# Optimization experiments

Measured on AMD Instinct MI355X. Metric: run time of the kernel, lower is better.

Reference implementation:

```python
import jax, jax.numpy as jnp
import numpy as np


def setup_inputs() -> dict:
    key = jax.random.key(0)
    x = jax.random.normal(key, (8, 512, 96, 96), dtype=jnp.float32)
    gamma = jnp.zeros((1,), dtype=jnp.float32)  # Scale(0) learnable scalar
    return {"x": x, "gamma": gamma}


def reference(x, gamma):
    b, c, h, w = x.shape
    y = x.reshape(b, c, h * w)                      # [B, C, N]
    # channel-channel Gram matrix: [B, C, C]
    att = jnp.einsum('bcn,bdn->bcd', y, y)
    # DANet variant: softmax of (rowmax - scores)
    att = jnp.max(att, axis=-1, keepdims=True) - att
    att = jax.nn.softmax(att, axis=-1)
    # attention-weighted aggregation over channels: [B, C, N]
    feat = jnp.einsum('bcd,bdn->bcn', att, y).reshape(b, c, h, w)
    return gamma * feat + x
```

## Files before the change

kernel.cpp:

```cpp
#include <hip/hip_runtime.h>


typedef __attribute__((ext_vector_type(8))) short short8;
typedef __attribute__((ext_vector_type(4))) float f32x4;

#define GT 128
#define BK 64
#define LDA 72
#define NSPLIT 8
#define FBSPLIT 4

__device__ inline unsigned short f2bf(float f) {
    unsigned u = __builtin_bit_cast(unsigned, f);
    u += 0x7fffu + ((u >> 16) & 1u);
    return (unsigned short)(u >> 16);
}
__device__ inline unsigned permpack(float a, float b) {
    return __builtin_amdgcn_perm(__builtin_bit_cast(unsigned, b),
                                 __builtin_bit_cast(unsigned, a), 0x07060302u);
}
__device__ inline void gload_lds16(const short* g, short* l) {
    __builtin_amdgcn_global_load_lds(
        (const __attribute__((address_space(1))) void*)(g),
        (__attribute__((address_space(3))) void*)(l), 16, 0, 0);
}

__global__ __launch_bounds__(256) void tobf16_kernel(const float* __restrict__ x,
                                                     short* __restrict__ ybf) {
    const size_t total = (size_t)8 * 512 * 9216 / 8;
    const size_t stride = (size_t)gridDim.x * 256;
    for (size_t i = (size_t)blockIdx.x * 256 + threadIdx.x; i < total; i += stride) {
        const float4 a = ((const float4*)x)[2 * i];
        const float4 b = ((const float4*)x)[2 * i + 1];
        uint4 pv;
        pv.x = permpack(a.x, a.y);
        pv.y = permpack(a.z, a.w);
        pv.z = permpack(b.x, b.y);
        pv.w = permpack(b.z, b.w);
        ((uint4*)ybf)[i] = pv;
    }
}

__global__ __launch_bounds__(256, 3) void gram_kernel2(const short* __restrict__ ybf,
                                                       float* __restrict__ att) {
    const int C = 512, N = 9216;
    __shared__ short As[GT * BK];
    __shared__ short Bs[GT * BK];
    const int pair = blockIdx.x;
    const int i_ = (pair < 4) ? 0 : (pair < 7) ? 1 : (pair < 9) ? 2 : 3;
    const int j_ = pair - ((i_ == 0) ? 0 : (i_ == 1) ? 3 : (i_ == 2) ? 5 : 6);
    const int split = blockIdx.y, batch = blockIdx.z;
    const int c0 = i_ * GT, d0 = j_ * GT;
    const short* Y = ybf + (size_t)batch * C * N;
    const int t = threadIdx.x;
    const int w = t >> 6, l = t & 63;
    const int mw = (w >> 1) * 64, nw = (w & 1) * 64;
    const int lr = l & 15, lq = l >> 4;

    f32x4 acc[4][4] = {};
    const int kw = N / NSPLIT;
    const int kbeg = split * kw;
    for (int k0 = kbeg; k0 < kbeg + kw; k0 += BK) {
        #pragma unroll
        for (int p = 0; p < 4; ++p) {
            const int u = t + p * 256;
            const int row = u >> 3;
            const int us = (u ^ row) & 7;
            gload_lds16(Y + (size_t)(c0 + row) * N + k0 + us * 8, &As[u * 8]);
        }
        #pragma unroll
        for (int p = 0; p < 4; ++p) {
            const int u = t + p * 256;
            const int row = u >> 3;
            const int us = (u ^ row) & 7;
            gload_lds16(Y + (size_t)(d0 + row) * N + k0 + us * 8, &Bs[u * 8]);
        }
        __syncthreads();
        #pragma unroll
        for (int h = 0; h < 2; ++h) {
            short8 af[4], bf[4];
            #pragma unroll
            for (int i = 0; i < 4; i++) {
                const int r = mw + i * 16 + lr;
                af[i] = *(short8*)&As[r * BK + (((h * 4 + lq) ^ (r & 7)) * 8)];
            }
            #pragma unroll
            for (int j = 0; j < 4; j++) {
                const int r = nw + j * 16 + lr;
                bf[j] = *(short8*)&Bs[r * BK + (((h * 4 + lq) ^ (r & 7)) * 8)];
            }
            #pragma unroll
            for (int i = 0; i < 4; i++)
                #pragma unroll
                for (int j = 0; j < 4; j++)
                    acc[i][j] = __builtin_amdgcn_mfma_f32_16x16x32_bf16(af[i], bf[j], acc[i][j], 0, 0, 0);
        }
        __syncthreads();
    }
    float* S = att + (size_t)batch * C * C;
    const bool mirror = (i_ != j_);
    #pragma unroll
    for (int i = 0; i < 4; i++)
        #pragma unroll
        for (int j = 0; j < 4; j++)
            #pragma unroll
            for (int r = 0; r < 4; r++) {
                const int row = c0 + mw + i * 16 + lq * 4 + r;
                const int col = d0 + nw + j * 16 + lr;
                const float v = acc[i][j][r];
                unsafeAtomicAdd(&S[(size_t)row * C + col], v);
                if (mirror) unsafeAtomicAdd(&S[(size_t)col * C + row], v);
            }
}

__global__ __launch_bounds__(256) void softmax_kernel(float* __restrict__ att) {
    const int C = 512;
    float* S = att + (size_t)blockIdx.x * C;
    const int t = threadIdx.x;
    const float v0 = S[t], v1 = S[t + 256];

    float mn = fminf(v0, v1);
    #pragma unroll
    for (int off = 32; off > 0; off >>= 1) mn = fminf(mn, __shfl_xor(mn, off));
    __shared__ float redmin[4];
    const int wid = t >> 6, lane = t & 63;
    if (lane == 0) redmin[wid] = mn;
    __syncthreads();
    mn = fminf(fminf(redmin[0], redmin[1]), fminf(redmin[2], redmin[3]));

    const float e0 = expf(mn - v0), e1 = expf(mn - v1);
    float s = e0 + e1;
    #pragma unroll
    for (int off = 32; off > 0; off >>= 1) s += __shfl_xor(s, off);
    __shared__ float redsum[4];
    if (lane == 0) redsum[wid] = s;
    __syncthreads();
    s = redsum[0] + redsum[1] + redsum[2] + redsum[3];

    const float inv = 1.0f / s;
    unsigned short* S16 = (unsigned short*)S;
    S16[t] = f2bf(e0 * inv);
    S16[t + 256] = f2bf(e1 * inv);
}

__global__ __launch_bounds__(256, 3) void feat_kernel2(const float* __restrict__ att,
                                                       const short* __restrict__ ybf,
                                                       const float* __restrict__ x,
                                                       const float* __restrict__ gamma,
                                                       float* __restrict__ out) {
    const int C = 512, N = 9216;
    __shared__ short As[GT * BK];
    __shared__ short Bs[GT * BK];
    const int b  = blockIdx.z;
    const int c0 = blockIdx.y * GT;
    const int n0 = blockIdx.x * GT;
    const short* Ab = (const short*)(att + (size_t)b * C * C);
    const short* Y = ybf + (size_t)b * C * N;
    const int t = threadIdx.x;
    const int w = t >> 6, l = t & 63;
    const int mw = (w >> 1) * 64, nw = (w & 1) * 64;
    const int lr = l & 15, lq = l >> 4;
    const int ng = t & 31, kg = t >> 5;

    f32x4 acc[4][4] = {};
    for (int k0 = 0; k0 < C; k0 += BK) {
        #pragma unroll
        for (int p = 0; p < 4; ++p) {
            const int u = t + p * 256;
            const int row = u >> 3;
            const int us = (u ^ row) & 7;
            gload_lds16(Ab + (size_t)(c0 + row) * 1024 + k0 + us * 8, &As[u * 8]);
        }
        {
            const short* pB = Y + (size_t)(k0 + kg * 8) * N + n0 + ng * 4;
            uint2 rr[8];
            #pragma unroll
            for (int r = 0; r < 8; ++r) rr[r] = *(const uint2*)(pB + (size_t)r * N);
            #pragma unroll
            for (int j = 0; j < 4; ++j) {
                const unsigned sel = (j & 1) ? 0x07060302u : 0x05040100u;
                unsigned w0, w1, w2, w3;
                if (j < 2) {
                    w0 = __builtin_amdgcn_perm(rr[1].x, rr[0].x, sel);
                    w1 = __builtin_amdgcn_perm(rr[3].x, rr[2].x, sel);
                    w2 = __builtin_amdgcn_perm(rr[5].x, rr[4].x, sel);
                    w3 = __builtin_amdgcn_perm(rr[7].x, rr[6].x, sel);
                } else {
                    w0 = __builtin_amdgcn_perm(rr[1].y, rr[0].y, sel);
                    w1 = __builtin_amdgcn_perm(rr[3].y, rr[2].y, sel);
                    w2 = __builtin_amdgcn_perm(rr[5].y, rr[4].y, sel);
                    w3 = __builtin_amdgcn_perm(rr[7].y, rr[6].y, sel);
                }
                const int nrow = ng * 4 + j;
                uint4 cv; cv.x = w0; cv.y = w1; cv.z = w2; cv.w = w3;
                *(uint4*)&Bs[nrow * BK + ((kg ^ (nrow & 7)) * 8)] = cv;
            }
        }
        __syncthreads();
        #pragma unroll
        for (int h = 0; h < 2; ++h) {
            short8 af[4], bf[4];
            #pragma unroll
            for (int i = 0; i < 4; i++) {
                const int r = mw + i * 16 + lr;
                af[i] = *(short8*)&As[r * BK + (((h * 4 + lq) ^ (r & 7)) * 8)];
            }
            #pragma unroll
            for (int j = 0; j < 4; j++) {
                const int r = nw + j * 16 + lr;
                bf[j] = *(short8*)&Bs[r * BK + (((h * 4 + lq) ^ (r & 7)) * 8)];
            }
            #pragma unroll
            for (int i = 0; i < 4; i++)
                #pragma unroll
                for (int j = 0; j < 4; j++)
                    acc[i][j] = __builtin_amdgcn_mfma_f32_16x16x32_bf16(af[i], bf[j], acc[i][j], 0, 0, 0);
        }
        __syncthreads();
    }

    const float g = gamma[0];
    float* O = out + (size_t)b * C * N;
    const float* X = x + (size_t)b * C * N;
    #pragma unroll
    for (int i = 0; i < 4; i++)
        #pragma unroll
        for (int j = 0; j < 4; j++)
            #pragma unroll
            for (int r = 0; r < 4; r++) {
                const int row = c0 + mw + i * 16 + lq * 4 + r;
                const int col = n0 + nw + j * 16 + lr;
                const size_t idx = (size_t)row * N + col;
                O[idx] = g * acc[i][j][r] + X[idx];
            }
}

__global__ __launch_bounds__(256, 2) void gram_fb(const float* __restrict__ x,
                                                  float* __restrict__ att,
                                                  int C, int N) {
    __shared__ short As[GT * LDA];
    __shared__ short Bs[GT * LDA];
    const int bz = blockIdx.z;
    const int batch = bz & 7, split = bz >> 3;
    const int c0 = blockIdx.y * GT;
    const int d0 = blockIdx.x * GT;
    const float* Y = x + (size_t)batch * C * N;
    const int t = threadIdx.x;
    const int w = t >> 6, l = t & 63;
    const int mw = (w >> 1) * 64, nw = (w & 1) * 64;
    const int lr = l & 15, lq = l >> 4;

    f32x4 acc[4][4] = {};
    const int kbeg = split * (N / FBSPLIT);
    const int kend = kbeg + (N / FBSPLIT);
    for (int k0 = kbeg; k0 < kend; k0 += BK) {
        #pragma unroll
        for (int i = 0; i < 8; i++) {
            const int v = t + i * 256;
            const int row = v >> 4, kq = v & 15;
            float4 a = *(const float4*)(Y + (size_t)(c0 + row) * N + k0 + kq * 4);
            uint2 pa = make_uint2(permpack(a.x, a.y), permpack(a.z, a.w));
            *(uint2*)&As[row * LDA + kq * 4] = pa;
            float4 bv = *(const float4*)(Y + (size_t)(d0 + row) * N + k0 + kq * 4);
            uint2 pb = make_uint2(permpack(bv.x, bv.y), permpack(bv.z, bv.w));
            *(uint2*)&Bs[row * LDA + kq * 4] = pb;
        }
        __syncthreads();
        #pragma unroll
        for (int h = 0; h < 2; h++) {
            short8 af[4], bf[4];
            #pragma unroll
            for (int i = 0; i < 4; i++)
                af[i] = *(short8*)&As[(mw + i * 16 + lr) * LDA + h * 32 + lq * 8];
            #pragma unroll
            for (int j = 0; j < 4; j++)
                bf[j] = *(short8*)&Bs[(nw + j * 16 + lr) * LDA + h * 32 + lq * 8];
            #pragma unroll
            for (int i = 0; i < 4; i++)
                #pragma unroll
                for (int j = 0; j < 4; j++)
                    acc[i][j] = __builtin_amdgcn_mfma_f32_16x16x32_bf16(af[i], bf[j], acc[i][j], 0, 0, 0);
        }
        __syncthreads();
    }
    float* S = att + (size_t)batch * C * C;
    #pragma unroll
    for (int i = 0; i < 4; i++)
        #pragma unroll
        for (int j = 0; j < 4; j++)
            #pragma unroll
            for (int r = 0; r < 4; r++) {
                const int row = c0 + mw + i * 16 + lq * 4 + r;
                const int col = d0 + nw + j * 16 + lr;
                unsafeAtomicAdd(&S[(size_t)row * C + col], acc[i][j][r]);
            }
}

__global__ __launch_bounds__(256, 2) void feat_fb(const float* __restrict__ att,
                                                  const float* __restrict__ x,
                                                  const float* __restrict__ gamma,
                                                  float* __restrict__ out,
                                                  int C, int N) {
    __shared__ short As[GT * LDA];
    __shared__ short Bs[GT * LDA];
    const int b  = blockIdx.z;
    const int c0 = blockIdx.y * GT;
    const int n0 = blockIdx.x * GT;
    const short* Ab = (const short*)(att + (size_t)b * C * C);
    const float* Y = x + (size_t)b * C * N;
    const int t = threadIdx.x;
    const int w = t >> 6, l = t & 63;
    const int mw = (w >> 1) * 64, nw = (w & 1) * 64;
    const int lr = l & 15, lq = l >> 4;

    f32x4 acc[4][4] = {};
    for (int k0 = 0; k0 < C; k0 += BK) {
        #pragma unroll
        for (int i = 0; i < 4; i++) {
            const int v = t + i * 256;
            const int row = v >> 3, q = v & 7;
            uint4 va = *(const uint4*)(Ab + (size_t)(c0 + row) * 1024 + k0 + q * 8);
            *(uint4*)&As[row * LDA + q * 8] = va;
        }
        #pragma unroll
        for (int i = 0; i < 2; i++) {
            const int v = t + i * 256;
            const int kg = v & 15, ng = v >> 4;
            const float* p0 = Y + (size_t)(k0 + kg * 4) * N + n0 + ng * 4;
            float4 r0 = *(const float4*)(p0);
            float4 r1 = *(const float4*)(p0 + N);
            float4 r2 = *(const float4*)(p0 + 2 * (size_t)N);
            float4 r3 = *(const float4*)(p0 + 3 * (size_t)N);
            const float j0[4] = {r0.x, r1.x, r2.x, r3.x};
            const float j1[4] = {r0.y, r1.y, r2.y, r3.y};
            const float j2[4] = {r0.z, r1.z, r2.z, r3.z};
            const float j3[4] = {r0.w, r1.w, r2.w, r3.w};
            const float* cols[4] = {j0, j1, j2, j3};
            #pragma unroll
            for (int j = 0; j < 4; j++) {
                uint2 p = make_uint2(permpack(cols[j][0], cols[j][1]),
                                     permpack(cols[j][2], cols[j][3]));
                *(uint2*)&Bs[(ng * 4 + j) * LDA + kg * 4] = p;
            }
        }
        __syncthreads();
        #pragma unroll
        for (int h = 0; h < 2; h++) {
            short8 af[4], bf[4];
            #pragma unroll
            for (int i = 0; i < 4; i++)
                af[i] = *(short8*)&As[(mw + i * 16 + lr) * LDA + h * 32 + lq * 8];
            #pragma unroll
            for (int j = 0; j < 4; j++)
                bf[j] = *(short8*)&Bs[(nw + j * 16 + lr) * LDA + h * 32 + lq * 8];
            #pragma unroll
            for (int i = 0; i < 4; i++)
                #pragma unroll
                for (int j = 0; j < 4; j++)
                    acc[i][j] = __builtin_amdgcn_mfma_f32_16x16x32_bf16(af[i], bf[j], acc[i][j], 0, 0, 0);
        }
        __syncthreads();
    }

    const float g = gamma[0];
    float* O = out + (size_t)b * C * N;
    const float* X = x + (size_t)b * C * N;
    #pragma unroll
    for (int i = 0; i < 4; i++)
        #pragma unroll
        for (int j = 0; j < 4; j++)
            #pragma unroll
            for (int r = 0; r < 4; r++) {
                const int row = c0 + mw + i * 16 + lq * 4 + r;
                const int col = n0 + nw + j * 16 + lr;
                const size_t idx = (size_t)row * N + col;
                O[idx] = g * acc[i][j][r] + X[idx];
            }
}

extern "C" void kernel_launch(void* const* d_in, const int* in_sizes, int n_in,
                              void* d_out, int out_size, void* d_ws, size_t ws_size,
                              hipStream_t stream) {
    const int B = 8, C = 512, N = 96 * 96;
    const float* x     = (const float*)d_in[0];
    const float* gamma = (const float*)d_in[1];
    float* out = (float*)d_out;
    float* att = (float*)d_ws;
    const size_t attBytes = (size_t)B * C * C * sizeof(float);
    const size_t ybfBytes = (size_t)B * C * N * sizeof(short);

    hipMemsetAsync(att, 0, attBytes, stream);

    dim3 blk(256);
    if (ws_size >= attBytes + ybfBytes) {
        short* ybf = (short*)((char*)d_ws + attBytes);
        tobf16_kernel<<<2048, blk, 0, stream>>>(x, ybf);
        gram_kernel2<<<dim3(10, NSPLIT, B), blk, 0, stream>>>(ybf, att);
        softmax_kernel<<<dim3(B * C), blk, 0, stream>>>(att);
        feat_kernel2<<<dim3(N / GT, C / GT, B), blk, 0, stream>>>(att, ybf, x, gamma, out);
    } else {
        gram_fb<<<dim3(C / GT, C / GT, B * FBSPLIT), blk, 0, stream>>>(x, att, C, N);
        softmax_kernel<<<dim3(B * C), blk, 0, stream>>>(att);
        feat_fb<<<dim3(N / GT, C / GT, B), blk, 0, stream>>>(att, x, gamma, out, C, N);
    }
}
```

Baseline: 482.7 us.

## Double-buffer LDS in gram and feat kernels, remap grids batch-interleaved

Both GEMM kernels now use two LDS buffers, so the global loads for the next K tile are issued while MFMAs run on the current tile. This replaces the old load, sync, compute, sync sequence. The gram kernel skips loading a separate B tile for diagonal blocks and reads A twice instead. Both grids are flattened, with batch as the fastest-varying index, to change block scheduling and cache locality. The cost is twice the LDS per block, and launch bounds drop from 3 to 2 blocks per SM, which lowers occupancy.

```diff
diff --git a/kernel.cpp b/kernel.cpp
--- a/kernel.cpp
+++ b/kernel.cpp
@@ -41,15 +41,19 @@
     }
 }
 
-__global__ __launch_bounds__(256, 3) void gram_kernel2(const short* __restrict__ ybf,
+__global__ __launch_bounds__(256, 2) void gram_kernel3(const short* __restrict__ ybf,
                                                        float* __restrict__ att) {
     const int C = 512, N = 9216;
-    __shared__ short As[GT * BK];
-    __shared__ short Bs[GT * BK];
-    const int pair = blockIdx.x;
+    __shared__ short As[2][GT * BK];
+    __shared__ short Bs[2][GT * BK];
+    const int id = blockIdx.x;
+    const int batch = id & 7;
+    const int slot = id >> 3;
+    const int split = slot / 10;
+    const int pair = slot % 10;
     const int i_ = (pair < 4) ? 0 : (pair < 7) ? 1 : (pair < 9) ? 2 : 3;
     const int j_ = pair - ((i_ == 0) ? 0 : (i_ == 1) ? 3 : (i_ == 2) ? 5 : 6);
-    const int split = blockIdx.y, batch = blockIdx.z;
+    const bool diag = (i_ == j_);
     const int c0 = i_ * GT, d0 = j_ * GT;
     const short* Y = ybf + (size_t)batch * C * N;
     const int t = threadIdx.x;
@@ -57,37 +61,50 @@
     const int mw = (w >> 1) * 64, nw = (w & 1) * 64;
     const int lr = l & 15, lq = l >> 4;
 
-    f32x4 acc[4][4] = {};
     const int kw = N / NSPLIT;
     const int kbeg = split * kw;
-    for (int k0 = kbeg; k0 < kbeg + kw; k0 += BK) {
+    const int nt = kw / BK;
+
+    auto STAGE = [&](int ti, int buf) {
+        const int k0 = kbeg + ti * BK;
         #pragma unroll
         for (int p = 0; p < 4; ++p) {
             const int u = t + p * 256;
             const int row = u >> 3;
             const int us = (u ^ row) & 7;
-            gload_lds16(Y + (size_t)(c0 + row) * N + k0 + us * 8, &As[u * 8]);
-        }
-        #pragma unroll
-        for (int p = 0; p < 4; ++p) {
-            const int u = t + p * 256;
-            const int row = u >> 3;
-            const int us = (u ^ row) & 7;
-            gload_lds16(Y + (size_t)(d0 + row) * N + k0 + us * 8, &Bs[u * 8]);
-        }
-        __syncthreads();
+            gload_lds16(Y + (size_t)(c0 + row) * N + k0 + us * 8, &As[buf][u * 8]);
+        }
+        if (!diag) {
+            #pragma unroll
+            for (int p = 0; p < 4; ++p) {
+                const int u = t + p * 256;
+                const int row = u >> 3;
+                const int us = (u ^ row) & 7;
+                gload_lds16(Y + (size_t)(d0 + row) * N + k0 + us * 8, &Bs[buf][u * 8]);
+            }
+        }
+    };
+
+    f32x4 acc[4][4] = {};
+    STAGE(0, 0);
+    __syncthreads();
+    int cur = 0;
+    for (int ti = 0; ti < nt; ++ti) {
+        if (ti + 1 < nt) STAGE(ti + 1, cur ^ 1);
+        const short* Acur = &As[cur][0];
+        const short* Bcur = diag ? &As[cur][0] : &Bs[cur][0];
         #pragma unroll
         for (int h = 0; h < 2; ++h) {
             short8 af[4], bf[4];
             #pragma unroll
             for (int i = 0; i < 4; i++) {
                 const int r = mw + i * 16 + lr;
-                af[i] = *(short8*)&As[r * BK + (((h * 4 + lq) ^ (r & 7)) * 8)];
+                af[i] = *(const short8*)&Acur[r * BK + (((h * 4 + lq) ^ (r & 7)) * 8)];
             }
             #pragma unroll
             for (int j = 0; j < 4; j++) {
                 const int r = nw + j * 16 + lr;
-                bf[j] = *(short8*)&Bs[r * BK + (((h * 4 + lq) ^ (r & 7)) * 8)];
+                bf[j] = *(const short8*)&Bcur[r * BK + (((h * 4 + lq) ^ (r & 7)) * 8)];
             }
             #pragma unroll
             for (int i = 0; i < 4; i++)
@@ -96,9 +113,9 @@
                     acc[i][j] = __builtin_amdgcn_mfma_f32_16x16x32_bf16(af[i], bf[j], acc[i][j], 0, 0, 0);
         }
         __syncthreads();
+        cur ^= 1;
     }
     float* S = att + (size_t)batch * C * C;
-    const bool mirror = (i_ != j_);
     #pragma unroll
     for (int i = 0; i < 4; i++)
         #pragma unroll
@@ -109,7 +126,7 @@
                 const int col = d0 + nw + j * 16 + lr;
                 const float v = acc[i][j][r];
                 unsafeAtomicAdd(&S[(size_t)row * C + col], v);
-                if (mirror) unsafeAtomicAdd(&S[(size_t)col * C + row], v);
+                if (!diag) unsafeAtomicAdd(&S[(size_t)col * C + row], v);
             }
 }
 
@@ -143,17 +160,19 @@
     S16[t + 256] = f2bf(e1 * inv);
 }
 
-__global__ __launch_bounds__(256, 3) void feat_kernel2(const float* __restrict__ att,
+__global__ __launch_bounds__(256, 2) void feat_kernel3(const float* __restrict__ att,
                                                        const short* __restrict__ ybf,
                                                        const float* __restrict__ x,
                                                        const float* __restrict__ gamma,
                                                        float* __restrict__ out) {
     const int C = 512, N = 9216;
-    __shared__ short As[GT * BK];
-    __shared__ short Bs[GT * BK];
-    const int b  = blockIdx.z;
-    const int c0 = blockIdx.y * GT;
-    const int n0 = blockIdx.x * GT;
+    __shared__ short As[2][GT * BK];
+    __shared__ short Bs[2][GT * BK];
+    const int id = blockIdx.x;
+    const int b = id & 7;
+    const int slot = id >> 3;
+    const int n0 = (slot >> 2) * GT;
+    const int c0 = (slot & 3) * GT;
     const short* Ab = (const short*)(att + (size_t)b * C * C);
     const short* Y = ybf + (size_t)b * C * N;
     const int t = threadIdx.x;
@@ -162,53 +181,70 @@
     const int lr = l & 15, lq = l >> 4;
     const int ng = t & 31, kg = t >> 5;
 
-    f32x4 acc[4][4] = {};
-    for (int k0 = 0; k0 < C; k0 += BK) {
+    const int nt = C / BK;
+
+    auto ASTAGE = [&](int ti, int buf) {
+        const int k0 = ti * BK;
         #pragma unroll
         for (int p = 0; p < 4; ++p) {
             const int u = t + p * 256;
             const int row = u >> 3;
             const int us = (u ^ row) & 7;
-            gload_lds16(Ab + (size_t)(c0 + row) * 1024 + k0 + us * 8, &As[u * 8]);
-        }
-        {
-            const short* pB = Y + (size_t)(k0 + kg * 8) * N + n0 + ng * 4;
-            uint2 rr[8];
-            #pragma unroll
-            for (int r = 0; r < 8; ++r) rr[r] = *(const uint2*)(pB + (size_t)r * N);
-            #pragma unroll
-            for (int j = 0; j < 4; ++j) {
-                const unsigned sel = (j & 1) ? 0x07060302u : 0x05040100u;
-                unsigned w0, w1, w2, w3;
-                if (j < 2) {
-                    w0 = __builtin_amdgcn_perm(rr[1].x, rr[0].x, sel);
-                    w1 = __builtin_amdgcn_perm(rr[3].x, rr[2].x, sel);
-                    w2 = __builtin_amdgcn_perm(rr[5].x, rr[4].x, sel);
-                    w3 = __builtin_amdgcn_perm(rr[7].x, rr[6].x, sel);
-                } else {
-                    w0 = __builtin_amdgcn_perm(rr[1].y, rr[0].y, sel);
-                    w1 = __builtin_amdgcn_perm(rr[3].y, rr[2].y, sel);
-                    w2 = __builtin_amdgcn_perm(rr[5].y, rr[4].y, sel);
-                    w3 = __builtin_amdgcn_perm(rr[7].y, rr[6].y, sel);
-                }
-                const int nrow = ng * 4 + j;
-                uint4 cv; cv.x = w0; cv.y = w1; cv.z = w2; cv.w = w3;
-                *(uint4*)&Bs[nrow * BK + ((kg ^ (nrow & 7)) * 8)] = cv;
-            }
-        }
-        __syncthreads();
+            gload_lds16(Ab + (size_t)(c0 + row) * 1024 + k0 + us * 8, &As[buf][u * 8]);
+        }
+    };
+
+    uint2 rr[8];
+    auto BLOAD = [&](int ti) {
+        const short* pB = Y + (size_t)(ti * BK + kg * 8) * N + n0 + ng * 4;
+        #pragma unroll
+        for (int r = 0; r < 8; ++r) rr[r] = *(const uint2*)(pB + (size_t)r * N);
+    };
+    auto BWRITE = [&](int buf) {
+        #pragma unroll
+        for (int j = 0; j < 4; ++j) {
+            const unsigned sel = (j & 1) ? 0x07060302u : 0x05040100u;
+            unsigned w0, w1, w2, w3;
+            if (j < 2) {
+                w0 = __builtin_amdgcn_perm(rr[1].x, rr[0].x, sel);
+                w1 = __builtin_amdgcn_perm(rr[3].x, rr[2].x, sel);
+                w2 = __builtin_amdgcn_perm(rr[5].x, rr[4].x, sel);
+                w3 = __builtin_amdgcn_perm(rr[7].x, rr[6].x, sel);
+            } else {
+                w0 = __builtin_amdgcn_perm(rr[1].y, rr[0].y, sel);
+                w1 = __builtin_amdgcn_perm(rr[3].y, rr[2].y, sel);
+                w2 = __builtin_amdgcn_perm(rr[5].y, rr[4].y, sel);
+                w3 = __builtin_amdgcn_perm(rr[7].y, rr[6].y, sel);
+            }
+            const int nrow = ng * 4 + j;
+            uint4 cv; cv.x = w0; cv.y = w1; cv.z = w2; cv.w = w3;
+            *(uint4*)&Bs[buf][nrow * BK + ((kg ^ (nrow & 7)) * 8)] = cv;
+        }
+    };
+
+    f32x4 acc[4][4] = {};
+    BLOAD(0);
+    ASTAGE(0, 0);
+    BWRITE(0);
+    __syncthreads();
+    int cur = 0;
+    for (int ti = 0; ti < nt; ++ti) {
+        if (ti + 1 < nt) {
+            BLOAD(ti + 1);
+            ASTAGE(ti + 1, cur ^ 1);
+        }
         #pragma unroll
         for (int h = 0; h < 2; ++h) {
             short8 af[4], bf[4];
             #pragma unroll
             for (int i = 0; i < 4; i++) {
                 const int r = mw + i * 16 + lr;
-                af[i] = *(short8*)&As[r * BK + (((h * 4 + lq) ^ (r & 7)) * 8)];
+                af[i] = *(const short8*)&As[cur][r * BK + (((h * 4 + lq) ^ (r & 7)) * 8)];
             }
             #pragma unroll
             for (int j = 0; j < 4; j++) {
                 const int r = nw + j * 16 + lr;
-                bf[j] = *(short8*)&Bs[r * BK + (((h * 4 + lq) ^ (r & 7)) * 8)];
+                bf[j] = *(const short8*)&Bs[cur][r * BK + (((h * 4 + lq) ^ (r & 7)) * 8)];
             }
             #pragma unroll
             for (int i = 0; i < 4; i++)
@@ -216,7 +252,9 @@
                 for (int j = 0; j < 4; j++)
                     acc[i][j] = __builtin_amdgcn_mfma_f32_16x16x32_bf16(af[i], bf[j], acc[i][j], 0, 0, 0);
         }
-        __syncthreads();
+        if (ti + 1 < nt) BWRITE(cur ^ 1);
+        __syncthreads();
+        cur ^= 1;
     }
 
     const float g = gamma[0];
@@ -395,9 +433,9 @@
     if (ws_size >= attBytes + ybfBytes) {
         short* ybf = (short*)((char*)d_ws + attBytes);
         tobf16_kernel<<<2048, blk, 0, stream>>>(x, ybf);
-        gram_kernel2<<<dim3(10, NSPLIT, B), blk, 0, stream>>>(ybf, att);
+        gram_kernel3<<<dim3(8 * NSPLIT * 10), blk, 0, stream>>>(ybf, att);
         softmax_kernel<<<dim3(B * C), blk, 0, stream>>>(att);
-        feat_kernel2<<<dim3(N / GT, C / GT, B), blk, 0, stream>>>(att, ybf, x, gamma, out);
+        feat_kernel3<<<dim3(8 * 288), blk, 0, stream>>>(att, ybf, x, gamma, out);
     } else {
         gram_fb<<<dim3(C / GT, C / GT, B * FBSPLIT), blk, 0, stream>>>(x, att, C, N);
         softmax_kernel<<<dim3(B * C), blk, 0, stream>>>(att);
```

Result: no change. 485.8 us (+0.7%).
